# Performance work log

Hardware: AMD Instinct MI355X
Metric: run time of the kernel (lower is better)

Reference implementation:

```python
import jax, jax.numpy as jnp
import numpy as np

NUM_NODES = 100000
NUM_EDGES = 1600000
IN_DIM = 128
OUT_DIM = 128


def setup_inputs() -> dict:
    key = jax.random.key(0)
    k_x, k_e, k_wn, k_bn, k_ws, k_bs = jax.random.split(key, 6)
    x = jax.random.normal(k_x, (NUM_NODES, IN_DIM), dtype=jnp.float32)
    edge_index = jax.random.randint(k_e, (2, NUM_EDGES), 0, NUM_NODES, dtype=jnp.int64)
    s = 1.0 / np.sqrt(IN_DIM)
    W_neigh = jax.random.uniform(k_wn, (OUT_DIM, IN_DIM), dtype=jnp.float32, minval=-s, maxval=s)
    b_neigh = jax.random.uniform(k_bn, (OUT_DIM,), dtype=jnp.float32, minval=-s, maxval=s)
    W_self = jax.random.uniform(k_ws, (OUT_DIM, IN_DIM), dtype=jnp.float32, minval=-s, maxval=s)
    b_self = jax.random.uniform(k_bs, (OUT_DIM,), dtype=jnp.float32, minval=-s, maxval=s)
    return {"x": x, "edge_index": edge_index, "W_neigh": W_neigh, "b_neigh": b_neigh,
            "W_self": W_self, "b_self": b_self}


def reference(x, edge_index, W_neigh, b_neigh, W_self, b_self):
    src, dst = edge_index[0], edge_index[1]
    # gather source node feats per edge, sum-aggregate per destination node
    msgs = x[src]  # [E, d]
    neigh = jax.ops.segment_sum(msgs, dst, num_segments=x.shape[0])  # [N, d]
    neigh_proj = neigh @ W_neigh.T + b_neigh  # [N, out]
    self_proj = x @ W_self.T + b_self         # [N, out]
    return neigh_proj + self_proj
```

## Files before the change

kernel.cpp:

```cpp
#include <hip/hip_runtime.h>
#include <hip/hip_bf16.h>

#define NN 100000
#define NE 1600000
#define DIM 128
#define BM 64
#define CAP 28
#define OVFCAP 131072
#define CVT_BLK 1024
#define SC_BLK 1024

typedef __attribute__((ext_vector_type(8))) short short8;
typedef __attribute__((ext_vector_type(4))) float f32x4;
typedef __attribute__((ext_vector_type(4))) unsigned short ushort4v;

__device__ __forceinline__ unsigned short f2bf(float f) {
  union { float f; unsigned u; } v; v.f = f;
  unsigned r = v.u + 0x7fffu + ((v.u >> 16) & 1u);
  return (unsigned short)(r >> 16);
}
__device__ __forceinline__ float bf2f(unsigned short h) {
  union { unsigned u; float f; } v; v.u = ((unsigned)h) << 16;
  return v.f;
}

__global__ __launch_bounds__(256) void prep_scatter_kernel(
    const float* __restrict__ x, const int* __restrict__ ei,
    const float* __restrict__ Wn, const float* __restrict__ bn,
    const float* __restrict__ Ws, const float* __restrict__ bs,
    unsigned short* __restrict__ xb, unsigned short* __restrict__ wnb,
    unsigned short* __restrict__ wsb, float* __restrict__ bsum,
    int* __restrict__ cnt, int* __restrict__ ovfcnt, int2* __restrict__ ovf,
    int* __restrict__ slots) {
  int b = blockIdx.x;
  if (b < CVT_BLK) {
    int tid = b * 256 + threadIdx.x;
    const int stride = CVT_BLK * 256;
    const int NC = NN * DIM / 4;
    for (int i = tid; i < NC; i += stride) {
      f32x4 v = reinterpret_cast<const f32x4*>(x)[i];
      ushort4v u;
      u[0] = f2bf(v[0]); u[1] = f2bf(v[1]); u[2] = f2bf(v[2]); u[3] = f2bf(v[3]);
      reinterpret_cast<ushort4v*>(xb)[i] = u;
    }
    if (tid < DIM * DIM) { wnb[tid] = f2bf(Wn[tid]); wsb[tid] = f2bf(Ws[tid]); }
    if (tid < DIM) bsum[tid] = bn[tid] + bs[tid];
  } else {
    int tid = (b - CVT_BLK) * 256 + threadIdx.x;
    const int stride = SC_BLK * 256;
    for (int e = tid; e < NE; e += stride) {
      int src = ei[e];
      int dst = ei[NE + e];
      if ((unsigned)src >= NN || (unsigned)dst >= NN) continue;
      int r = atomicAdd(&cnt[dst], 1);
      if (r < CAP) {
        slots[dst * CAP + r] = src;
      } else {
        int o = atomicAdd(ovfcnt, 1);
        if (o < OVFCAP) ovf[o] = make_int2(dst, src);
      }
    }
  }
}

__global__ __launch_bounds__(512) void fusedgemm_kernel(
    const unsigned short* __restrict__ xb,
    const int* __restrict__ cnt, const int* __restrict__ slots,
    const int2* __restrict__ ovf, const int* __restrict__ ovfcnt,
    const unsigned short* __restrict__ wnb, const unsigned short* __restrict__ wsb,
    const float* __restrict__ bsum, float* __restrict__ out) {
  __shared__ unsigned short sW[DIM * DIM];
  __shared__ unsigned short sA[BM * DIM];
  __shared__ unsigned short sX[BM * DIM];
  __shared__ int2 lovf[256];
  __shared__ int lovfn;
  const int tid = threadIdx.x;
  const int row0 = blockIdx.x * BM;

  if (tid == 0) lovfn = 0;
  #pragma unroll
  for (int it = 0; it < 2; ++it) {
    int id = it * 512 + tid;
    int r = id >> 4, c = id & 15;
    int gr = row0 + r;
    short8 v = (short8)0;
    if (gr < NN) v = *reinterpret_cast<const short8*>(xb + (size_t)gr * DIM + c * 8);
    int off = (r * 256 + c * 16) ^ ((r & 7) << 4);
    *reinterpret_cast<short8*>(reinterpret_cast<char*>(sX) + off) = v;
  }
  #pragma unroll
  for (int it = 0; it < 4; ++it) {
    int id = it * 512 + tid;
    int r = id >> 4, c = id & 15;
    short8 w = *reinterpret_cast<const short8*>(wnb + r * DIM + c * 8);
    int off = (r * 256 + c * 16) ^ ((r & 7) << 4);
    *reinterpret_cast<short8*>(reinterpret_cast<char*>(sW) + off) = w;
  }
  __syncthreads();

  {
    int ovfn = min(*ovfcnt, OVFCAP);
    for (int k = tid; k < ovfn; k += 512) {
      int2 p = ovf[k];
      if ((unsigned)(p.x - row0) < (unsigned)BM) {
        int t = atomicAdd(&lovfn, 1);
        if (t < 256) lovf[t] = p;
      }
    }
  }
  __syncthreads();

  {
    const int lg = tid >> 5, ln = tid & 31;
    int g = row0 + lg;
    int m = 0, idx = 0;
    if (g < NN) {
      m = min(cnt[g], CAP);
      if (ln < m) idx = slots[g * CAP + ln];
    }
    const int lcnt = min(lovfn, 256);
    for (int it = 0; it < 4; ++it) {
      int r = it * 16 + lg;
      int gcur = row0 + r;
      int mn = 0, idxn = 0;
      if (it < 3) {
        int gn = row0 + (it + 1) * 16 + lg;
        if (gn < NN) {
          mn = min(cnt[gn], CAP);
          if (ln < mn) idxn = slots[gn * CAP + ln];
        }
      }
      f32x4 a0 = (f32x4){0.f,0.f,0.f,0.f}, a1 = a0, a2 = a0, a3 = a0;
      f32x4 a4 = a0, a5 = a0, a6 = a0, a7 = a0;
      int e = 0;
      for (; e + 7 < m; e += 8) {
        int s0 = __shfl(idx, e, 32),     s1 = __shfl(idx, e + 1, 32);
        int s2 = __shfl(idx, e + 2, 32), s3 = __shfl(idx, e + 3, 32);
        int s4 = __shfl(idx, e + 4, 32), s5 = __shfl(idx, e + 5, 32);
        int s6 = __shfl(idx, e + 6, 32), s7 = __shfl(idx, e + 7, 32);
        ushort4v u0 = *reinterpret_cast<const ushort4v*>(xb + (size_t)s0 * DIM + ln * 4);
        ushort4v u1 = *reinterpret_cast<const ushort4v*>(xb + (size_t)s1 * DIM + ln * 4);
        ushort4v u2 = *reinterpret_cast<const ushort4v*>(xb + (size_t)s2 * DIM + ln * 4);
        ushort4v u3 = *reinterpret_cast<const ushort4v*>(xb + (size_t)s3 * DIM + ln * 4);
        ushort4v u4 = *reinterpret_cast<const ushort4v*>(xb + (size_t)s4 * DIM + ln * 4);
        ushort4v u5 = *reinterpret_cast<const ushort4v*>(xb + (size_t)s5 * DIM + ln * 4);
        ushort4v u6 = *reinterpret_cast<const ushort4v*>(xb + (size_t)s6 * DIM + ln * 4);
        ushort4v u7 = *reinterpret_cast<const ushort4v*>(xb + (size_t)s7 * DIM + ln * 4);
        #pragma unroll
        for (int j = 0; j < 4; ++j) {
          a0[j] += bf2f(u0[j]); a1[j] += bf2f(u1[j]);
          a2[j] += bf2f(u2[j]); a3[j] += bf2f(u3[j]);
          a4[j] += bf2f(u4[j]); a5[j] += bf2f(u5[j]);
          a6[j] += bf2f(u6[j]); a7[j] += bf2f(u7[j]);
        }
      }
      for (; e + 3 < m; e += 4) {
        int s0 = __shfl(idx, e, 32),     s1 = __shfl(idx, e + 1, 32);
        int s2 = __shfl(idx, e + 2, 32), s3 = __shfl(idx, e + 3, 32);
        ushort4v u0 = *reinterpret_cast<const ushort4v*>(xb + (size_t)s0 * DIM + ln * 4);
        ushort4v u1 = *reinterpret_cast<const ushort4v*>(xb + (size_t)s1 * DIM + ln * 4);
        ushort4v u2 = *reinterpret_cast<const ushort4v*>(xb + (size_t)s2 * DIM + ln * 4);
        ushort4v u3 = *reinterpret_cast<const ushort4v*>(xb + (size_t)s3 * DIM + ln * 4);
        #pragma unroll
        for (int j = 0; j < 4; ++j) {
          a0[j] += bf2f(u0[j]); a1[j] += bf2f(u1[j]);
          a2[j] += bf2f(u2[j]); a3[j] += bf2f(u3[j]);
        }
      }
      for (; e < m; ++e) {
        int s0 = __shfl(idx, e, 32);
        ushort4v u0 = *reinterpret_cast<const ushort4v*>(xb + (size_t)s0 * DIM + ln * 4);
        #pragma unroll
        for (int j = 0; j < 4; ++j) a0[j] += bf2f(u0[j]);
      }
      for (int k2 = 0; k2 < lcnt; ++k2) {
        int2 p = lovf[k2];
        if (p.x == gcur) {
          ushort4v u0 = *reinterpret_cast<const ushort4v*>(xb + (size_t)p.y * DIM + ln * 4);
          #pragma unroll
          for (int j = 0; j < 4; ++j) a0[j] += bf2f(u0[j]);
        }
      }
      a0 += a1; a2 += a3; a4 += a5; a6 += a7;
      a0 += a2; a4 += a6; a0 += a4;
      ushort4v o;
      o[0] = f2bf(a0[0]); o[1] = f2bf(a0[1]); o[2] = f2bf(a0[2]); o[3] = f2bf(a0[3]);
      int off = (r * 256 + ln * 8) ^ ((r & 7) << 4);
      *reinterpret_cast<ushort4v*>(reinterpret_cast<char*>(sA) + off) = o;
      idx = idxn; m = mn;
    }
  }
  __syncthreads();

  const int wave = tid >> 6;
  const int lane = tid & 63;
  const int wm = wave & 3, wn = wave >> 2;
  const int arow = wm * 16 + (lane & 15);
  const int kl = (lane >> 4) * 8;
  f32x4 acc[4];
  #pragma unroll
  for (int t = 0; t < 4; ++t) acc[t] = (f32x4){0.f, 0.f, 0.f, 0.f};

  #pragma unroll
  for (int ks = 0; ks < 4; ++ks) {
    int k = ks * 32 + kl;
    short8 a = *reinterpret_cast<const short8*>(
        reinterpret_cast<const char*>(sA) + ((arow * 256 + k * 2) ^ ((arow & 7) << 4)));
    #pragma unroll
    for (int t = 0; t < 4; ++t) {
      int o = (wn * 4 + t) * 16 + (lane & 15);
      short8 bfr = *reinterpret_cast<const short8*>(
          reinterpret_cast<const char*>(sW) + ((o * 256 + k * 2) ^ ((o & 7) << 4)));
      acc[t] = __builtin_amdgcn_mfma_f32_16x16x32_bf16(a, bfr, acc[t], 0, 0, 0);
    }
  }
  __syncthreads();
  #pragma unroll
  for (int it = 0; it < 4; ++it) {
    int id = it * 512 + tid;
    int r = id >> 4, c = id & 15;
    short8 w = *reinterpret_cast<const short8*>(wsb + r * DIM + c * 8);
    int off = (r * 256 + c * 16) ^ ((r & 7) << 4);
    *reinterpret_cast<short8*>(reinterpret_cast<char*>(sW) + off) = w;
  }
  __syncthreads();
  #pragma unroll
  for (int ks = 0; ks < 4; ++ks) {
    int k = ks * 32 + kl;
    short8 a = *reinterpret_cast<const short8*>(
        reinterpret_cast<const char*>(sX) + ((arow * 256 + k * 2) ^ ((arow & 7) << 4)));
    #pragma unroll
    for (int t = 0; t < 4; ++t) {
      int o = (wn * 4 + t) * 16 + (lane & 15);
      short8 bfr = *reinterpret_cast<const short8*>(
          reinterpret_cast<const char*>(sW) + ((o * 256 + k * 2) ^ ((o & 7) << 4)));
      acc[t] = __builtin_amdgcn_mfma_f32_16x16x32_bf16(a, bfr, acc[t], 0, 0, 0);
    }
  }

  #pragma unroll
  for (int t = 0; t < 4; ++t) {
    int col = (wn * 4 + t) * 16 + (lane & 15);
    float bv = bsum[col];
    #pragma unroll
    for (int reg = 0; reg < 4; ++reg) {
      int gr = row0 + wm * 16 + (lane >> 4) * 4 + reg;
      if (gr < NN) out[(size_t)gr * DIM + col] = acc[t][reg] + bv;
    }
  }
}

extern "C" void kernel_launch(void* const* d_in, const int* in_sizes, int n_in,
                              void* d_out, int out_size, void* d_ws, size_t ws_size,
                              hipStream_t stream) {
  const float* x  = (const float*)d_in[0];
  const int*   ei = (const int*)d_in[1];
  const float* Wn = (const float*)d_in[2];
  const float* bn = (const float*)d_in[3];
  const float* Ws = (const float*)d_in[4];
  const float* bs = (const float*)d_in[5];
  float* out = (float*)d_out;
  char* ws = (char*)d_ws;

  unsigned short* wnb = (unsigned short*)(ws + 0);
  unsigned short* wsb = (unsigned short*)(ws + 32768);
  float* bsum        = (float*)(ws + 65536);
  int* cnt           = (int*)(ws + 66560);
  int* ovfcnt        = (int*)(ws + 466560);
  int2* ovf          = (int2*)(ws + 466688);
  int* slots         = (int*)(ws + 1515264);
  unsigned short* xb = (unsigned short*)(ws + 12715264);

  hipMemsetAsync(cnt, 0, 400064, stream);
  prep_scatter_kernel<<<CVT_BLK + SC_BLK, 256, 0, stream>>>(
      x, ei, Wn, bn, Ws, bs, xb, wnb, wsb, bsum, cnt, ovfcnt, ovf, slots);
  fusedgemm_kernel<<<(NN + BM - 1) / BM, 512, 0, stream>>>(
      xb, cnt, slots, ovf, ovfcnt, wnb, wsb, bsum, out);
}
```

Measured before the change: 193.4 us.

## Partition edge scatter by destination range and pad counters to reduce atomic contention

The scatter blocks are split into 8 groups. Each group handles one destination range of 12500 nodes, so a given node's slots and counter are touched by only one group, which should improve locality. Every block now reads the whole dst array and filters it, so dst reads grow eightfold. Per-node counters are padded to a stride of 4 ints to spread atomics across cache lines, the x-to-bf16 conversion uses nontemporal loads and stores, and the overflow capacity shrinks, which risks dropping edges for high-degree nodes.

```diff
diff --git a/kernel.cpp b/kernel.cpp
--- a/kernel.cpp
+++ b/kernel.cpp
@@ -6,9 +6,11 @@
 #define DIM 128
 #define BM 64
 #define CAP 28
-#define OVFCAP 131072
+#define OVFCAP 16384
 #define CVT_BLK 1024
 #define SC_BLK 1024
+#define CSTRIDE 4
+#define XRANGE 12500
 
 typedef __attribute__((ext_vector_type(8))) short short8;
 typedef __attribute__((ext_vector_type(4))) float f32x4;
@@ -38,26 +40,41 @@
     const int stride = CVT_BLK * 256;
     const int NC = NN * DIM / 4;
     for (int i = tid; i < NC; i += stride) {
-      f32x4 v = reinterpret_cast<const f32x4*>(x)[i];
+      f32x4 v = __builtin_nontemporal_load(reinterpret_cast<const f32x4*>(x) + i);
       ushort4v u;
       u[0] = f2bf(v[0]); u[1] = f2bf(v[1]); u[2] = f2bf(v[2]); u[3] = f2bf(v[3]);
-      reinterpret_cast<ushort4v*>(xb)[i] = u;
+      __builtin_nontemporal_store(u, reinterpret_cast<ushort4v*>(xb) + i);
     }
     if (tid < DIM * DIM) { wnb[tid] = f2bf(Wn[tid]); wsb[tid] = f2bf(Ws[tid]); }
     if (tid < DIM) bsum[tid] = bn[tid] + bs[tid];
   } else {
-    int tid = (b - CVT_BLK) * 256 + threadIdx.x;
-    const int stride = SC_BLK * 256;
-    for (int e = tid; e < NE; e += stride) {
-      int src = ei[e];
-      int dst = ei[NE + e];
-      if ((unsigned)src >= NN || (unsigned)dst >= NN) continue;
-      int r = atomicAdd(&cnt[dst], 1);
-      if (r < CAP) {
-        slots[dst * CAP + r] = src;
-      } else {
-        int o = atomicAdd(ovfcnt, 1);
-        if (o < OVFCAP) ovf[o] = make_int2(dst, src);
+    const int sb  = b - CVT_BLK;
+    const int lo  = (sb & 7) * XRANGE;
+    const int gr  = sb >> 3;
+    const int tid_g = gr * 256 + threadIdx.x;
+    const int STR = 128 * 256;
+    for (int e0 = tid_g; e0 < NE; e0 += 4 * STR) {
+      int dj[4];
+      #pragma unroll
+      for (int j = 0; j < 4; ++j) {
+        int ee = e0 + j * STR;
+        dj[j] = (ee < NE) ? __builtin_nontemporal_load(ei + NE + ee) : -1;
+      }
+      #pragma unroll
+      for (int j = 0; j < 4; ++j) {
+        if ((unsigned)(dj[j] - lo) < (unsigned)XRANGE) {
+          int ee = e0 + j * STR;
+          int s = ei[ee];
+          if ((unsigned)s >= NN) continue;
+          int d = dj[j];
+          int r = atomicAdd(&cnt[d * CSTRIDE], 1);
+          if (r < CAP) {
+            slots[d * CAP + r] = s;
+          } else {
+            int o = atomicAdd(ovfcnt, 1);
+            if (o < OVFCAP) ovf[o] = make_int2(d, s);
+          }
+        }
       }
     }
   }
@@ -115,7 +132,7 @@
     int g = row0 + lg;
     int m = 0, idx = 0;
     if (g < NN) {
-      m = min(cnt[g], CAP);
+      m = min(cnt[g * CSTRIDE], CAP);
       if (ln < m) idx = slots[g * CAP + ln];
     }
     const int lcnt = min(lovfn, 256);
@@ -126,7 +143,7 @@
       if (it < 3) {
         int gn = row0 + (it + 1) * 16 + lg;
         if (gn < NN) {
-          mn = min(cnt[gn], CAP);
+          mn = min(cnt[gn * CSTRIDE], CAP);
           if (ln < mn) idxn = slots[gn * CAP + ln];
         }
       }
@@ -266,12 +283,12 @@
   unsigned short* wsb = (unsigned short*)(ws + 32768);
   float* bsum        = (float*)(ws + 65536);
   int* cnt           = (int*)(ws + 66560);
-  int* ovfcnt        = (int*)(ws + 466560);
-  int2* ovf          = (int2*)(ws + 466688);
-  int* slots         = (int*)(ws + 1515264);
-  unsigned short* xb = (unsigned short*)(ws + 12715264);
-
-  hipMemsetAsync(cnt, 0, 400064, stream);
+  int* ovfcnt        = (int*)(ws + 1666560);
+  int2* ovf          = (int2*)(ws + 1666624);
+  int* slots         = (int*)(ws + 1797696);
+  unsigned short* xb = (unsigned short*)(ws + 12997696);
+
+  hipMemsetAsync(cnt, 0, 1600064, stream);
   prep_scatter_kernel<<<CVT_BLK + SC_BLK, 256, 0, stream>>>(
       x, ei, Wn, bn, Ws, bs, xb, wnb, wsb, bsum, cnt, ovfcnt, ovf, slots);
   fusedgemm_kernel<<<(NN + BM - 1) / BM, 512, 0, stream>>>(
```

Measured after the change: 205.0 us. 1.06x slower.
